# Kernel tuning notes

Measured on AMD Instinct MI355X. Metric: run time of the kernel, lower is better.

Reference implementation:

```python
import jax, jax.numpy as jnp
import numpy as np

N_NODES = 100000
N_EDGES = 1600000
D_IN = 128
D_HID = 64
BN_EPS = 1e-5


def setup_inputs() -> dict:
    key = jax.random.key(0)
    ks = jax.random.split(key, 8)
    x = jax.random.normal(ks[0], (N_NODES, D_IN), dtype=jnp.float32)
    edge_index = jax.random.randint(ks[1], (2, N_EDGES), 0, N_NODES, dtype=jnp.int64)
    # GCNConv1 weight/bias (glorot-ish scale)
    W1 = jax.random.normal(ks[2], (D_IN, D_HID), dtype=jnp.float32) / np.sqrt(D_IN)
    b1 = jnp.zeros((D_HID,), dtype=jnp.float32)
    # BatchNorm1d (eval mode: running stats)
    gamma = jax.random.normal(ks[3], (D_HID,), dtype=jnp.float32) * 0.1 + 1.0
    beta = jax.random.normal(ks[4], (D_HID,), dtype=jnp.float32) * 0.1
    run_mean = jnp.zeros((D_HID,), dtype=jnp.float32)
    run_var = jnp.ones((D_HID,), dtype=jnp.float32)
    # fc1: Linear(2*hidden, 2)
    Wfc = jax.random.normal(ks[5], (2 * D_HID, 2), dtype=jnp.float32) / np.sqrt(2 * D_HID)
    bfc = jnp.zeros((2,), dtype=jnp.float32)
    return {"x": x, "edge_index": edge_index, "W1": W1, "b1": b1,
            "gamma": gamma, "beta": beta, "run_mean": run_mean, "run_var": run_var,
            "Wfc": Wfc, "bfc": bfc}


def gcn_conv(x, edge_index, W, b):
    # PyG GCNConv: add self-loops, symmetric normalization, scatter-add aggregation
    n = x.shape[0]
    loops = jnp.arange(n, dtype=edge_index.dtype)
    row = jnp.concatenate([edge_index[0], loops])  # source nodes
    col = jnp.concatenate([edge_index[1], loops])  # target nodes
    deg = jax.ops.segment_sum(jnp.ones_like(col, dtype=x.dtype), col, num_segments=n)
    dinv = jax.lax.rsqrt(jnp.maximum(deg, 1.0))  # deg >= 1 due to self-loops
    norm = dinv[row] * dinv[col]                 # [E+N]
    h = x @ W                                    # [N, hid]
    msgs = h[row] * norm[:, None]                # gather + scale  [E+N, hid]
    out = jax.ops.segment_sum(msgs, col, num_segments=n)  # scatter-add
    return out + b


def reference(x, edge_index, W1, b1, gamma, beta, run_mean, run_var, Wfc, bfc):
    h = gcn_conv(x, edge_index, W1, b1)
    h = jax.nn.relu(h)
    # dropout(p=0.9) is identity in eval mode
    # BatchNorm1d eval: normalize with running stats
    h = (h - run_mean) * jax.lax.rsqrt(run_var + BN_EPS) * gamma + beta
    h = jax.nn.relu(h)
    # edge gather-concat-linear
    er = jnp.concatenate([h[edge_index[0]], h[edge_index[1]]], axis=1)  # [E, 2*hid]
    return er @ Wfc + bfc  # [E, 2]
```

## Files before the change

### kernel.cpp

```cpp
#include <hip/hip_runtime.h>

#define N_NODES 100000
#define N_EDGES 1600000
#define D_IN 128
#define D_HID 64
#define BN_EPS 1e-5f

#define BUCKET_SHIFT 7
#define BUCKET_W 128
#define N_BUCKETS ((N_NODES + BUCKET_W - 1) / BUCKET_W)
#define BCAP 4096
#define N_BIN_BLOCKS 250
#define EDGES_PER_BLOCK (N_EDGES / N_BIN_BLOCKS)
#define E4_PER_BLOCK (EDGES_PER_BLOCK / 4)
#define GT 5

typedef __attribute__((ext_vector_type(8))) short bf16x8;
typedef __attribute__((ext_vector_type(4))) float f32x4;
typedef __attribute__((ext_vector_type(8))) _Float16 f16x8;

__device__ __forceinline__ ushort f2bf(float f) {
    unsigned u = __float_as_uint(f);
    u += 0x7FFF + ((u >> 16) & 1);
    return (ushort)(u >> 16);
}

__global__ __launch_bounds__(1024) void bin_scatter_kernel(const int* __restrict__ row,
                                                           const int* __restrict__ col,
                                                           int* __restrict__ bcursor,
                                                           int* __restrict__ binned) {
    __shared__ int hist[N_BUCKETS];
    __shared__ int lbase[N_BUCKETS];
    const int t = threadIdx.x;
    for (int i = t; i < N_BUCKETS; i += 1024) hist[i] = 0;
    __syncthreads();
    const int e0 = blockIdx.x * EDGES_PER_BLOCK;
    const int4* __restrict__ colv = (const int4*)(col + e0);
    const int4* __restrict__ rowv = (const int4*)(row + e0);
    for (int j4 = t; j4 < E4_PER_BLOCK; j4 += 1024) {
        int4 c = colv[j4];
        atomicAdd(&hist[c.x >> BUCKET_SHIFT], 1);
        atomicAdd(&hist[c.y >> BUCKET_SHIFT], 1);
        atomicAdd(&hist[c.z >> BUCKET_SHIFT], 1);
        atomicAdd(&hist[c.w >> BUCKET_SHIFT], 1);
    }
    __syncthreads();
    for (int i = t; i < N_BUCKETS; i += 1024) {
        int h = hist[i];
        lbase[i] = h ? (i * BCAP + atomicAdd(&bcursor[i], h)) : 0;
        hist[i] = 0;
    }
    __syncthreads();
    for (int j4 = t; j4 < E4_PER_BLOCK; j4 += 1024) {
        int4 c = colv[j4];
        int4 r = rowv[j4];
        int cc[4] = {c.x, c.y, c.z, c.w};
        int rr[4] = {r.x, r.y, r.z, r.w};
        #pragma unroll
        for (int k = 0; k < 4; ++k) {
            int b = cc[k] >> BUCKET_SHIFT;
            int rank = atomicAdd(&hist[b], 1);
            binned[lbase[b] + rank] = ((cc[k] & (BUCKET_W - 1)) << 17) | rr[k];
        }
    }
}

__global__ __launch_bounds__(512) void bucket_csr_kernel(const int* __restrict__ binned,
                                                         const int* __restrict__ bcursor,
                                                         int* __restrict__ csr_src,
                                                         int2* __restrict__ rs2,
                                                         float* __restrict__ dinv) {
    __shared__ int eb[BCAP];
    __shared__ int cl[BCAP];
    __shared__ int hist[BUCKET_W];
    __shared__ int cursor[BUCKET_W];
    const int b = blockIdx.x;
    const int t = threadIdx.x;
    if (t < BUCKET_W) hist[t] = 0;
    __syncthreads();
    const int s = b * BCAP;
    const int cnt = bcursor[b];
    const int n4 = (cnt + 3) >> 2;
    const int4* __restrict__ binv = (const int4*)(binned + s);
    for (int i4 = t; i4 < n4; i4 += 512) {
        int4 v = binv[i4];
        int vv[4] = {v.x, v.y, v.z, v.w};
        #pragma unroll
        for (int k = 0; k < 4; ++k) {
            int idx = 4 * i4 + k;
            if (idx < cnt) {
                eb[idx] = vv[k];
                atomicAdd(&hist[vv[k] >> 17], 1);
            }
        }
    }
    __syncthreads();
    if (t < BUCKET_W) cursor[t] = hist[t];
    for (int off = 1; off < BUCKET_W; off <<= 1) {
        __syncthreads();
        int add = (t >= off && t < BUCKET_W) ? cursor[t - off] : 0;
        __syncthreads();
        if (t < BUCKET_W) cursor[t] += add;
    }
    __syncthreads();
    int excl = (t < BUCKET_W) ? (cursor[t] - hist[t]) : 0;
    __syncthreads();
    if (t < BUCKET_W) cursor[t] = excl;
    const int node = b * BUCKET_W + t;
    if (t < BUCKET_W && node < N_NODES) {
        rs2[node] = make_int2(s + excl, hist[t]);
        dinv[node] = rsqrtf(1.0f + (float)hist[t]);
    }
    __syncthreads();
    for (int i = t; i < cnt; i += 512) {
        int p = eb[i];
        int pos = atomicAdd(&cursor[p >> 17], 1);
        cl[pos] = p & 0x1FFFF;
    }
    __syncthreads();
    int4* __restrict__ csrv = (int4*)(csr_src + s);
    const int4* __restrict__ clv = (const int4*)cl;
    for (int i4 = t; i4 < n4; i4 += 512)
        csrv[i4] = clv[i4];
}

__global__ __launch_bounds__(256) void gemm_mfma_kernel(const float* __restrict__ x,
                                                        const float* __restrict__ W,
                                                        const float* __restrict__ dinv,
                                                        ushort* __restrict__ h_s) {
    __shared__ ushort xb[16 * 136];
    const int t = threadIdx.x;
    const int l = t & 63;
    const int wv = t >> 6;
    const int q = l >> 4;
    const int m = l & 15;
    bf16x8 bf[4];
    {
        const int n = wv * 16 + m;
        #pragma unroll
        for (int s = 0; s < 4; ++s)
            #pragma unroll
            for (int j = 0; j < 8; ++j)
                bf[s][j] = (short)f2bf(W[(32 * s + 8 * q + j) * D_HID + n]);
    }
    for (int tile = 0; tile < GT; ++tile) {
        const int node0 = blockIdx.x * (16 * GT) + tile * 16;
        __syncthreads();
        for (int i = t; i < 512; i += 256) {
            int r = i >> 5, c4 = i & 31;
            float4 v = *(const float4*)&x[(size_t)(node0 + r) * D_IN + c4 * 4];
            ushort4 u = make_ushort4(f2bf(v.x), f2bf(v.y), f2bf(v.z), f2bf(v.w));
            *(ushort4*)&xb[r * 136 + c4 * 4] = u;
        }
        __syncthreads();
        f32x4 acc = {0.f, 0.f, 0.f, 0.f};
        #pragma unroll
        for (int s = 0; s < 4; ++s) {
            bf16x8 af = *(const bf16x8*)&xb[m * 136 + 32 * s + 8 * q];
            acc = __builtin_amdgcn_mfma_f32_16x16x32_bf16(af, bf[s], acc, 0, 0, 0);
        }
        #pragma unroll
        for (int r = 0; r < 4; ++r) {
            int node = node0 + q * 4 + r;
            _Float16 hv = (_Float16)(acc[r] * dinv[node]);
            h_s[node * D_HID + wv * 16 + m] = __builtin_bit_cast(unsigned short, hv);
        }
    }
}

__global__ __launch_bounds__(256) void aggregate_kernel(const ushort* __restrict__ h_s,
                                                        const float* __restrict__ dinv,
                                                        const int2* __restrict__ rs2,
                                                        const int* __restrict__ csr_src,
                                                        const float* __restrict__ b1,
                                                        const float* __restrict__ gamma,
                                                        const float* __restrict__ beta,
                                                        const float* __restrict__ mean,
                                                        const float* __restrict__ var,
                                                        const float* __restrict__ Wfc,
                                                        float4* __restrict__ uv) {
    const f16x8* __restrict__ hsv = (const f16x8*)h_s;
    const int wvid = (blockIdx.x * 256 + threadIdx.x) >> 6;
    const int lane = threadIdx.x & 63;
    const int oct = lane >> 3;
    const int ol = lane & 7;
    const int n = wvid * 8 + oct;
    f16x8 acc = hsv[n * 8 + ol];
    const int2 rs = rs2[n];
    const int start = rs.x;
    const int cnt = rs.y;
    int j = 0;
    for (; j + 8 <= cnt; j += 8) {
        int i0 = csr_src[start + j + 0];
        int i1 = csr_src[start + j + 1];
        int i2 = csr_src[start + j + 2];
        int i3 = csr_src[start + j + 3];
        int i4 = csr_src[start + j + 4];
        int i5 = csr_src[start + j + 5];
        int i6 = csr_src[start + j + 6];
        int i7 = csr_src[start + j + 7];
        f16x8 v0 = hsv[i0 * 8 + ol];
        f16x8 v1 = hsv[i1 * 8 + ol];
        f16x8 v2 = hsv[i2 * 8 + ol];
        f16x8 v3 = hsv[i3 * 8 + ol];
        f16x8 v4 = hsv[i4 * 8 + ol];
        f16x8 v5 = hsv[i5 * 8 + ol];
        f16x8 v6 = hsv[i6 * 8 + ol];
        f16x8 v7 = hsv[i7 * 8 + ol];
        acc += v0; acc += v1; acc += v2; acc += v3;
        acc += v4; acc += v5; acc += v6; acc += v7;
    }
    for (; j + 4 <= cnt; j += 4) {
        int i0 = csr_src[start + j + 0];
        int i1 = csr_src[start + j + 1];
        int i2 = csr_src[start + j + 2];
        int i3 = csr_src[start + j + 3];
        f16x8 v0 = hsv[i0 * 8 + ol];
        f16x8 v1 = hsv[i1 * 8 + ol];
        f16x8 v2 = hsv[i2 * 8 + ol];
        f16x8 v3 = hsv[i3 * 8 + ol];
        acc += v0; acc += v1; acc += v2; acc += v3;
    }
    for (; j + 2 <= cnt; j += 2) {
        int i0 = csr_src[start + j + 0];
        int i1 = csr_src[start + j + 1];
        f16x8 v0 = hsv[i0 * 8 + ol];
        f16x8 v1 = hsv[i1 * 8 + ol];
        acc += v0; acc += v1;
    }
    if (j < cnt)
        acc += hsv[csr_src[start + j] * 8 + ol];
    const float dn = dinv[n];
    const int f0 = 8 * ol;
    float a[8];
    #pragma unroll
    for (int k = 0; k < 8; ++k) a[k] = (float)acc[k] * dn;
    float bb[8], mu[8], vr[8], gm[8], bt[8];
    *(float4*)&bb[0] = *(const float4*)&b1[f0];    *(float4*)&bb[4] = *(const float4*)&b1[f0 + 4];
    *(float4*)&mu[0] = *(const float4*)&mean[f0];  *(float4*)&mu[4] = *(const float4*)&mean[f0 + 4];
    *(float4*)&vr[0] = *(const float4*)&var[f0];   *(float4*)&vr[4] = *(const float4*)&var[f0 + 4];
    *(float4*)&gm[0] = *(const float4*)&gamma[f0]; *(float4*)&gm[4] = *(const float4*)&gamma[f0 + 4];
    *(float4*)&bt[0] = *(const float4*)&beta[f0];  *(float4*)&bt[4] = *(const float4*)&beta[f0 + 4];
    #pragma unroll
    for (int k = 0; k < 8; ++k) {
        float v = fmaxf(a[k] + bb[k], 0.f);
        a[k] = fmaxf((v - mu[k]) * rsqrtf(vr[k] + BN_EPS) * gm[k] + bt[k], 0.f);
    }
    float wt[16], wb[16];
    #pragma unroll
    for (int k = 0; k < 4; ++k) {
        *(float4*)&wt[4 * k] = *(const float4*)&Wfc[2 * f0 + 4 * k];
        *(float4*)&wb[4 * k] = *(const float4*)&Wfc[128 + 2 * f0 + 4 * k];
    }
    float p0 = 0.f, p1 = 0.f, p2 = 0.f, p3 = 0.f;
    #pragma unroll
    for (int k = 0; k < 8; ++k) {
        p0 += a[k] * wt[2 * k];
        p1 += a[k] * wt[2 * k + 1];
        p2 += a[k] * wb[2 * k];
        p3 += a[k] * wb[2 * k + 1];
    }
    #pragma unroll
    for (int off = 4; off > 0; off >>= 1) {
        p0 += __shfl_xor(p0, off, 64);
        p1 += __shfl_xor(p1, off, 64);
        p2 += __shfl_xor(p2, off, 64);
        p3 += __shfl_xor(p3, off, 64);
    }
    if (ol == 0) uv[n] = make_float4(p0, p1, p2, p3);
}

__global__ __launch_bounds__(256) void edgeout_kernel(const int* __restrict__ row,
                                                      const int* __restrict__ col,
                                                      const float4* __restrict__ uv,
                                                      const float* __restrict__ bfc,
                                                      float2* __restrict__ out) {
    int i = blockIdx.x * 256 + threadIdx.x;
    int e = i * 2;
    int2 rr = *(const int2*)&row[e];
    int2 cc = *(const int2*)&col[e];
    float4 a0 = uv[rr.x];
    float4 b0 = uv[cc.x];
    float4 a1 = uv[rr.y];
    float4 b1 = uv[cc.y];
    float c0 = bfc[0], c1 = bfc[1];
    float4 o = make_float4(a0.x + b0.z + c0, a0.y + b0.w + c1,
                           a1.x + b1.z + c0, a1.y + b1.w + c1);
    *(float4*)&out[e] = o;
}

extern "C" void kernel_launch(void* const* d_in, const int* in_sizes, int n_in,
                              void* d_out, int out_size, void* d_ws, size_t ws_size,
                              hipStream_t stream) {
    const float* x     = (const float*)d_in[0];
    const int*   ei    = (const int*)d_in[1];
    const int*   row   = ei;
    const int*   col   = ei + N_EDGES;
    const float* W1    = (const float*)d_in[2];
    const float* b1    = (const float*)d_in[3];
    const float* gamma = (const float*)d_in[4];
    const float* beta  = (const float*)d_in[5];
    const float* mean  = (const float*)d_in[6];
    const float* var   = (const float*)d_in[7];
    const float* Wfc   = (const float*)d_in[8];
    const float* bfc   = (const float*)d_in[9];
    float2* out = (float2*)d_out;

    char* ws = (char*)d_ws;
    size_t off = 0;
    ushort* h_s      = (ushort*)(ws + off); off += (size_t)N_NODES * D_HID * 2;
    int*   binned    = (int*)(ws + off);    off += (size_t)N_BUCKETS * BCAP * 4;
    int*   csr_src   = (int*)(ws + off);    off += (size_t)N_BUCKETS * BCAP * 4;
    int*   bcursor   = (int*)(ws + off);    off += ((size_t)N_BUCKETS * 4 + 15) & ~(size_t)15;
    int2*  rs2       = (int2*)(ws + off);   off += (size_t)N_NODES * 8;
    float* dinv      = (float*)(ws + off);  off += (size_t)N_NODES * 4;
    float4* uv       = (float4*)(ws + off); off += (size_t)N_NODES * 16;

    hipMemsetAsync(bcursor, 0, N_BUCKETS * sizeof(int), stream);
    bin_scatter_kernel<<<N_BIN_BLOCKS, 1024, 0, stream>>>(row, col, bcursor, binned);
    bucket_csr_kernel<<<N_BUCKETS, 512, 0, stream>>>(binned, bcursor, csr_src, rs2, dinv);
    gemm_mfma_kernel<<<N_NODES / (16 * GT), 256, 0, stream>>>(x, W1, dinv, h_s);
    aggregate_kernel<<<N_NODES / 32, 256, 0, stream>>>(h_s, dinv, rs2, csr_src,
                                                       b1, gamma, beta, mean, var,
                                                       Wfc, uv);
    edgeout_kernel<<<N_EDGES / 512, 256, 0, stream>>>(row, col, uv, bfc, out);
}
```

Before: 190.5 us.

## Fuse bucket CSR construction with the feature GEMM in one kernel

Merges the per-bucket CSR build and the x@W1 MFMA GEMM into one kernel, one block per 128-node bucket. The GEMM reuses the CSR shared memory through a union and reads each node's degree normalisation from shared memory instead of global dinv. Each block runs 4 rounds, with its two 256-thread halves each handling 16 nodes per round. This removes one kernel launch and the global dinv round trip, but the GEMM now waits on the CSR phase inside each block and the block's shared-memory footprint grows.

```diff
diff --git a/kernel.cpp b/kernel.cpp
--- a/kernel.cpp
+++ b/kernel.cpp
@@ -13,7 +13,6 @@
 #define N_BIN_BLOCKS 250
 #define EDGES_PER_BLOCK (N_EDGES / N_BIN_BLOCKS)
 #define E4_PER_BLOCK (EDGES_PER_BLOCK / 4)
-#define GT 5
 
 typedef __attribute__((ext_vector_type(8))) short bf16x8;
 typedef __attribute__((ext_vector_type(4))) float f32x4;
@@ -65,17 +64,39 @@
     }
 }
 
-__global__ __launch_bounds__(512) void bucket_csr_kernel(const int* __restrict__ binned,
-                                                         const int* __restrict__ bcursor,
-                                                         int* __restrict__ csr_src,
-                                                         int2* __restrict__ rs2,
-                                                         float* __restrict__ dinv) {
-    __shared__ int eb[BCAP];
-    __shared__ int cl[BCAP];
+union CsrGemmSh {
+    struct { int eb[BCAP]; int cl[BCAP]; } s;
+    ushort xb[2][16 * 136];
+};
+__global__ __launch_bounds__(512) void csr_gemm_kernel(const int* __restrict__ binned,
+                                                       const int* __restrict__ bcursor,
+                                                       const float* __restrict__ x,
+                                                       const float* __restrict__ W,
+                                                       int* __restrict__ csr_src,
+                                                       int2* __restrict__ rs2,
+                                                       float* __restrict__ dinv,
+                                                       ushort* __restrict__ h_s) {
+    __shared__ CsrGemmSh sh;
     __shared__ int hist[BUCKET_W];
     __shared__ int cursor[BUCKET_W];
+    __shared__ float dsh[BUCKET_W];
     const int b = blockIdx.x;
     const int t = threadIdx.x;
+
+    const int l = t & 63;
+    const int wv = (t >> 6) & 3;
+    const int q = l >> 4;
+    const int m = l & 15;
+    bf16x8 bf[4];
+    {
+        const int n = wv * 16 + m;
+        #pragma unroll
+        for (int s = 0; s < 4; ++s)
+            #pragma unroll
+            for (int j = 0; j < 8; ++j)
+                bf[s][j] = (short)f2bf(W[(32 * s + 8 * q + j) * D_HID + n]);
+    }
+
     if (t < BUCKET_W) hist[t] = 0;
     __syncthreads();
     const int s = b * BCAP;
@@ -89,7 +110,7 @@
         for (int k = 0; k < 4; ++k) {
             int idx = 4 * i4 + k;
             if (idx < cnt) {
-                eb[idx] = vv[k];
+                sh.s.eb[idx] = vv[k];
                 atomicAdd(&hist[vv[k] >> 17], 1);
             }
         }
@@ -106,64 +127,60 @@
     int excl = (t < BUCKET_W) ? (cursor[t] - hist[t]) : 0;
     __syncthreads();
     if (t < BUCKET_W) cursor[t] = excl;
-    const int node = b * BUCKET_W + t;
-    if (t < BUCKET_W && node < N_NODES) {
-        rs2[node] = make_int2(s + excl, hist[t]);
-        dinv[node] = rsqrtf(1.0f + (float)hist[t]);
+    {
+        const int node = b * BUCKET_W + t;
+        if (t < BUCKET_W) {
+            float dn = rsqrtf(1.0f + (float)hist[t]);
+            dsh[t] = dn;
+            if (node < N_NODES) {
+                rs2[node] = make_int2(s + excl, hist[t]);
+                dinv[node] = dn;
+            }
+        }
     }
     __syncthreads();
     for (int i = t; i < cnt; i += 512) {
-        int p = eb[i];
+        int p = sh.s.eb[i];
         int pos = atomicAdd(&cursor[p >> 17], 1);
-        cl[pos] = p & 0x1FFFF;
-    }
-    __syncthreads();
-    int4* __restrict__ csrv = (int4*)(csr_src + s);
-    const int4* __restrict__ clv = (const int4*)cl;
-    for (int i4 = t; i4 < n4; i4 += 512)
-        csrv[i4] = clv[i4];
-}
-
-__global__ __launch_bounds__(256) void gemm_mfma_kernel(const float* __restrict__ x,
-                                                        const float* __restrict__ W,
-                                                        const float* __restrict__ dinv,
-                                                        ushort* __restrict__ h_s) {
-    __shared__ ushort xb[16 * 136];
-    const int t = threadIdx.x;
-    const int l = t & 63;
-    const int wv = t >> 6;
-    const int q = l >> 4;
-    const int m = l & 15;
-    bf16x8 bf[4];
+        sh.s.cl[pos] = p & 0x1FFFF;
+    }
+    __syncthreads();
     {
-        const int n = wv * 16 + m;
-        #pragma unroll
-        for (int s = 0; s < 4; ++s)
-            #pragma unroll
-            for (int j = 0; j < 8; ++j)
-                bf[s][j] = (short)f2bf(W[(32 * s + 8 * q + j) * D_HID + n]);
-    }
-    for (int tile = 0; tile < GT; ++tile) {
-        const int node0 = blockIdx.x * (16 * GT) + tile * 16;
+        int4* __restrict__ csrv = (int4*)(csr_src + s);
+        const int4* __restrict__ clv = (const int4*)sh.s.cl;
+        for (int i4 = t; i4 < n4; i4 += 512)
+            csrv[i4] = clv[i4];
+    }
+    __syncthreads();
+
+    const int h = t >> 8;
+    const int tt = t & 255;
+    #pragma unroll
+    for (int rnd = 0; rnd < 4; ++rnd) {
+        const int node0 = b * BUCKET_W + rnd * 32 + h * 16;
         __syncthreads();
-        for (int i = t; i < 512; i += 256) {
+        for (int i = tt; i < 512; i += 256) {
             int r = i >> 5, c4 = i & 31;
-            float4 v = *(const float4*)&x[(size_t)(node0 + r) * D_IN + c4 * 4];
+            int nr = node0 + r;
+            if (nr >= N_NODES) nr = N_NODES - 1;
+            float4 v = *(const float4*)&x[(size_t)nr * D_IN + c4 * 4];
             ushort4 u = make_ushort4(f2bf(v.x), f2bf(v.y), f2bf(v.z), f2bf(v.w));
-            *(ushort4*)&xb[r * 136 + c4 * 4] = u;
+            *(ushort4*)&sh.xb[h][r * 136 + c4 * 4] = u;
         }
         __syncthreads();
         f32x4 acc = {0.f, 0.f, 0.f, 0.f};
         #pragma unroll
-        for (int s = 0; s < 4; ++s) {
-            bf16x8 af = *(const bf16x8*)&xb[m * 136 + 32 * s + 8 * q];
-            acc = __builtin_amdgcn_mfma_f32_16x16x32_bf16(af, bf[s], acc, 0, 0, 0);
+        for (int ks = 0; ks < 4; ++ks) {
+            bf16x8 af = *(const bf16x8*)&sh.xb[h][m * 136 + 32 * ks + 8 * q];
+            acc = __builtin_amdgcn_mfma_f32_16x16x32_bf16(af, bf[ks], acc, 0, 0, 0);
         }
         #pragma unroll
         for (int r = 0; r < 4; ++r) {
             int node = node0 + q * 4 + r;
-            _Float16 hv = (_Float16)(acc[r] * dinv[node]);
-            h_s[node * D_HID + wv * 16 + m] = __builtin_bit_cast(unsigned short, hv);
+            if (node < N_NODES) {
+                _Float16 hv = (_Float16)(acc[r] * dsh[node - b * BUCKET_W]);
+                h_s[node * D_HID + wv * 16 + m] = __builtin_bit_cast(unsigned short, hv);
+            }
         }
     }
 }
@@ -318,8 +335,8 @@
 
     hipMemsetAsync(bcursor, 0, N_BUCKETS * sizeof(int), stream);
     bin_scatter_kernel<<<N_BIN_BLOCKS, 1024, 0, stream>>>(row, col, bcursor, binned);
-    bucket_csr_kernel<<<N_BUCKETS, 512, 0, stream>>>(binned, bcursor, csr_src, rs2, dinv);
-    gemm_mfma_kernel<<<N_NODES / (16 * GT), 256, 0, stream>>>(x, W1, dinv, h_s);
+    csr_gemm_kernel<<<N_BUCKETS, 512, 0, stream>>>(binned, bcursor, x, W1,
+                                                   csr_src, rs2, dinv, h_s);
     aggregate_kernel<<<N_NODES / 32, 256, 0, stream>>>(h_s, dinv, rs2, csr_src,
                                                        b1, gamma, beta, mean, var,
                                                        Wfc, uv);
```

Result: no change. 188.1 us (-1.3%).
